# Performance work log

Measured on AMD Instinct MI355X. Metric: run time of the kernel, lower is better.

Reference implementation:

```python
import jax, jax.numpy as jnp
import numpy as np

KH, KW = 3, 3
DH, DW = 1, 1
H_OUT, W_OUT = 64, 64


def setup_inputs() -> dict:
    key = jax.random.key(0)
    k1, k2, k3 = jax.random.split(key, 3)
    x = jax.random.normal(k1, (32, 16, 66, 66), dtype=jnp.float32)
    # per-location (locally-connected) weights: [1, C_out, C_in, H_out, W_out, kh*kw]
    weight = jax.random.normal(k2, (1, 32, 16, 64, 64, 9), dtype=jnp.float32) * 0.1
    bias = jax.random.normal(k3, (1, 32, 64, 64), dtype=jnp.float32) * 0.1
    return {"x": x, "weight": weight, "bias": bias}


def _unfold(x):
    # torch x.unfold(2,kh,dh).unfold(3,kw,dw).view(B,C,Ho,Wo,kh*kw):
    # kernel index order is (i over kh, then j over kw).
    patches = jnp.stack(
        [x[:, :, i : i + H_OUT * DH : DH, j : j + W_OUT * DW : DW]
         for i in range(KH) for j in range(KW)],
        axis=-1,
    )  # [B, C_in, H_out, W_out, kh*kw]
    return patches


def reference(x, weight, bias):
    patches = _unfold(x)  # [B, C_in, Ho, Wo, K]
    # (x.unsqueeze(1) * weight).sum([2, -1]) == contraction over C_in and kernel,
    # with per-(h,w) unique weights; einsum avoids the huge 6D intermediate.
    out = jnp.einsum("bchwk,ochwk->bohw", patches, weight[0])
    out = out + bias  # bias has leading 1 batch dim, broadcasts
    return out
```

## Files before the change

kernel.cpp:

```cpp
#include <hip/hip_runtime.h>


#define CI_ 16
#define H_  64
#define W_  64
#define XW_ 66

typedef float f32x16 __attribute__((ext_vector_type(16)));
typedef short s16x8  __attribute__((ext_vector_type(8)));

__device__ inline short f2bf(float f) {
  unsigned u = __builtin_bit_cast(unsigned, f);
  u += 0x7fffu + ((u >> 16) & 1u);
  return (short)(u >> 16);
}

__device__ inline void gload_lds16(const float* g, void* l) {
  __builtin_amdgcn_global_load_lds(
      (const __attribute__((address_space(1))) void*)g,
      (__attribute__((address_space(3))) void*)l, 16, 0, 0);
}

__global__ __launch_bounds__(256) void prep_x(const float* __restrict__ x,
                                              short* __restrict__ xP) {
  const int t = blockIdx.x * 256 + threadIdx.x;
  const int oct = t & 1;
  const int b   = (t >> 1) & 31;
  const int hhww = t >> 6;
  const float* sp = x + ((size_t)b * CI_ + oct * 8) * 4356 + hhww;
  s16x8 v;
#pragma unroll
  for (int e = 0; e < 8; ++e) v[e] = f2bf(sp[(size_t)e * 4356]);
  *(s16x8*)(xP + (size_t)t * 8) = v;
}

__global__ __launch_bounds__(256) void lc2d_fused(
    const short* __restrict__ xP, const float* __restrict__ wt,
    const float* __restrict__ bias, float* __restrict__ out) {
  __shared__ float wlin[16 * 32 * 36];

  const int d = blockIdx.x;
  const int L = (d & 7) * 128 + (d >> 3);
  const int wq = L & 15;
  const int h  = L >> 4;
  const int tx = threadIdx.x;
  const int w2 = threadIdx.y;
  const int tid = w2 * 64 + tx;
  const int ln   = tx & 31;
  const int half = tx >> 5;
  const int w = wq * 4 + w2;

  const short* ap0 = xP + ln * 16 + half * 8;
  s16x8 af[9];
#pragma unroll
  for (int kk = 0; kk < 9; ++kk) {
    const int i = kk / 3, j = kk - 3 * i;
    af[kk] = *(const s16x8*)(ap0 + (size_t)((h + i) * XW_ + (w + j)) * 512);
  }

#pragma unroll
  for (int i = 0; i < 18; ++i) {
    const int G = i * 256 + tid;
    const int segL = G / 9;
    const int q    = G - 9 * segL;
    const int o = segL & 31, c = segL >> 5;
    const float* src = wt +
        (((size_t)(o * 16 + c) * 9216 + (size_t)h * 144 + wq * 9 + q) << 2);
    gload_lds16(src, (char*)wlin + (size_t)(i * 256 + w2 * 64) * 16);
  }
  __syncthreads();

  f32x16 acc = {0,0,0,0,0,0,0,0,0,0,0,0,0,0,0,0};
  const int bbase = half * 9216 + ln * 36 + w2 * 9;
#pragma unroll
  for (int kk = 0; kk < 9; ++kk) {
    s16x8 bf;
#pragma unroll
    for (int e = 0; e < 8; ++e) {
      bf[e] = f2bf(wlin[bbase + e * 1152 + kk]);
    }
    acc = __builtin_amdgcn_mfma_f32_32x32x16_bf16(af[kk], bf, acc, 0, 0, 0);
  }

  __syncthreads();
  float* tr = (float*)wlin;
#pragma unroll
  for (int r = 0; r < 16; ++r) {
    const int b = (r & 3) + 8 * (r >> 2) + 4 * half;
    tr[(w2 * 32 + b) * 32 + ln] = acc[r];
  }
  __syncthreads();

  const int o = tid & 31;
  const int brow = tid >> 5;
  const float4 bv = *(const float4*)(bias + ((size_t)o * H_ + h) * W_ + wq * 4);
#pragma unroll
  for (int it = 0; it < 4; ++it) {
    const int b = it * 8 + brow;
    float4 v;
    v.x = tr[(0 * 32 + b) * 32 + o] + bv.x;
    v.y = tr[(1 * 32 + b) * 32 + o] + bv.y;
    v.z = tr[(2 * 32 + b) * 32 + o] + bv.z;
    v.w = tr[(3 * 32 + b) * 32 + o] + bv.w;
    *(float4*)(out + ((size_t)b * 32 + o) * (H_ * W_) + h * W_ + wq * 4) = v;
  }
}

__global__ __launch_bounds__(256, 4) void lc2d_mfma0(
    const float* __restrict__ xs, const float* __restrict__ wt,
    const float* __restrict__ bias, float* __restrict__ out) {
  __shared__ float wlds[8 * 32 * 36];
  const int d = blockIdx.x;
  const int L = (d & 7) * 128 + (d >> 3);
  const int wq = L & 15;
  const int h  = L >> 4;
  const int tx = threadIdx.x;
  const int w2 = threadIdx.y;
  const int ln = tx & 31;
  const int half = tx >> 5;
  const int tid = w2 * 64 + tx;
  const int w = wq * 4 + w2;
  f32x16 acc = {0,0,0,0,0,0,0,0,0,0,0,0,0,0,0,0};
  const int bbase = ln * 36 + w2 * 9;
  size_t abase = (size_t)ln * 69696 + (size_t)h * XW_ + w;

  for (int s = 0; s < 2; ++s) {
    const int c0 = s * 8;
    __syncthreads();
#pragma unroll
    for (int i = 0; i < 9; ++i) {
      const int f4 = tid + i * 256;
      const int cc = f4 / 288;
      const int rem = f4 - cc * 288;
      const int oo = rem / 9;
      const int q = rem - oo * 9;
      const float4* src = (const float4*)wt +
          (((size_t)oo * CI_ + (c0 + cc)) * H_ + h) * 144 + (size_t)wq * 9 + q;
      ((float4*)wlds)[f4] = *src;
    }
    __syncthreads();
#pragma unroll
    for (int cc = 0; cc < 8; ++cc) {
      const int c = c0 + cc;
      const float* ap = xs + abase + (size_t)c * 4356;
      float av[8] = {0,0,0,0,0,0,0,0};
      float bvv[8] = {0,0,0,0,0,0,0,0};
      av[0] = ap[half ? (2 * XW_ + 2) : 0];
      bvv[0] = wlds[cc * 1152 + bbase + (half ? 8 : 0)];
      if (half == 0) {
#pragma unroll
        for (int e = 1; e < 8; ++e) {
          const int i = e / 3, j = e - 3 * i;
          av[e] = ap[i * XW_ + j];
          bvv[e] = wlds[cc * 1152 + bbase + e];
        }
      }
      s16x8 afr, bfr;
#pragma unroll
      for (int e = 0; e < 8; ++e) { afr[e] = f2bf(av[e]); bfr[e] = f2bf(bvv[e]); }
      acc = __builtin_amdgcn_mfma_f32_32x32x16_bf16(afr, bfr, acc, 0, 0, 0);
    }
  }
  const float bvv = bias[((size_t)ln * H_ + h) * W_ + w];
#pragma unroll
  for (int r = 0; r < 16; ++r) {
    const int b = (r & 3) + 8 * (r >> 2) + 4 * half;
    out[(((size_t)b * 32 + ln) * H_ + h) * W_ + w] = acc[r] + bvv;
  }
}

extern "C" void kernel_launch(void* const* d_in, const int* in_sizes, int n_in,
                              void* d_out, int out_size, void* d_ws, size_t ws_size,
                              hipStream_t stream) {
  const float* x    = (const float*)d_in[0];
  const float* wt   = (const float*)d_in[1];
  const float* bias = (const float*)d_in[2];
  float* out = (float*)d_out;

  const size_t xp_bytes = (size_t)66 * 66 * 32 * 16 * sizeof(short);
  if (ws_size >= xp_bytes) {
    short* xP = (short*)d_ws;
    prep_x<<<1089, 256, 0, stream>>>(x, xP);
    lc2d_fused<<<1024, dim3(64, 4, 1), 0, stream>>>(xP, wt, bias, out);
  } else {
    lc2d_mfma0<<<1024, dim3(64, 4, 1), 0, stream>>>(x, wt, bias, out);
  }
}
```

Measured before the change: 39.62 us.

## Process two output rows per block with double-buffered weight prefetch

Each block now handles two output rows (h and h+4) instead of one, and the grid is halved to match. All global and async-to-LDS loads for both rows are issued up front into two separate LDS buffers. A partial vmcnt wait then releases compute on the first row while the second row's loads are still in flight, so the second row's memory latency overlaps the first row's MFMA work and stores. In exchange LDS use roughly doubles to about 147KB per block, which limits each CU to one resident block and removes inter-block latency hiding.

```diff
diff --git a/kernel.cpp b/kernel.cpp
--- a/kernel.cpp
+++ b/kernel.cpp
@@ -37,12 +37,13 @@
 __global__ __launch_bounds__(256) void lc2d_fused(
     const short* __restrict__ xP, const float* __restrict__ wt,
     const float* __restrict__ bias, float* __restrict__ out) {
-  __shared__ float wlin[16 * 32 * 36];
+  __shared__ float pw[2][18432];
 
   const int d = blockIdx.x;
-  const int L = (d & 7) * 128 + (d >> 3);
-  const int wq = L & 15;
-  const int h  = L >> 4;
+  const int L0 = (d & 7) * 128 + (d >> 3);
+  const int wq = L0 & 15;
+  const int h0 = L0 >> 4;
+  const int h1 = h0 + 4;
   const int tx = threadIdx.x;
   const int w2 = threadIdx.y;
   const int tid = w2 * 64 + tx;
@@ -51,13 +52,14 @@
   const int w = wq * 4 + w2;
 
   const short* ap0 = xP + ln * 16 + half * 8;
-  s16x8 af[9];
+
+  s16x8 af0[9], af1[9];
 #pragma unroll
   for (int kk = 0; kk < 9; ++kk) {
     const int i = kk / 3, j = kk - 3 * i;
-    af[kk] = *(const s16x8*)(ap0 + (size_t)((h + i) * XW_ + (w + j)) * 512);
-  }
-
+    af0[kk] = *(const s16x8*)(ap0 + (size_t)((h0 + i) * XW_ + (w + j)) * 512);
+  }
+  __builtin_amdgcn_sched_barrier(0);
 #pragma unroll
   for (int i = 0; i < 18; ++i) {
     const int G = i * 256 + tid;
@@ -65,44 +67,100 @@
     const int q    = G - 9 * segL;
     const int o = segL & 31, c = segL >> 5;
     const float* src = wt +
-        (((size_t)(o * 16 + c) * 9216 + (size_t)h * 144 + wq * 9 + q) << 2);
-    gload_lds16(src, (char*)wlin + (size_t)(i * 256 + w2 * 64) * 16);
-  }
-  __syncthreads();
+        (((size_t)(o * 16 + c) * 9216 + (size_t)h0 * 144 + wq * 9 + q) << 2);
+    gload_lds16(src, (char*)&pw[0][0] + (size_t)(i * 256 + w2 * 64) * 16);
+  }
+  __builtin_amdgcn_sched_barrier(0);
+#pragma unroll
+  for (int kk = 0; kk < 9; ++kk) {
+    const int i = kk / 3, j = kk - 3 * i;
+    af1[kk] = *(const s16x8*)(ap0 + (size_t)((h1 + i) * XW_ + (w + j)) * 512);
+  }
+  __builtin_amdgcn_sched_barrier(0);
+#pragma unroll
+  for (int i = 0; i < 18; ++i) {
+    const int G = i * 256 + tid;
+    const int segL = G / 9;
+    const int q    = G - 9 * segL;
+    const int o = segL & 31, c = segL >> 5;
+    const float* src = wt +
+        (((size_t)(o * 16 + c) * 9216 + (size_t)h1 * 144 + wq * 9 + q) << 2);
+    gload_lds16(src, (char*)&pw[1][0] + (size_t)(i * 256 + w2 * 64) * 16);
+  }
+  __builtin_amdgcn_sched_barrier(0);
+
+  asm volatile("s_waitcnt vmcnt(27)" ::: "memory");
+  __builtin_amdgcn_sched_barrier(0);
+  __builtin_amdgcn_s_barrier();
+  __builtin_amdgcn_sched_barrier(0);
+
+  const int bbase = half * 9216 + ln * 36 + w2 * 9;
 
   f32x16 acc = {0,0,0,0,0,0,0,0,0,0,0,0,0,0,0,0};
-  const int bbase = half * 9216 + ln * 36 + w2 * 9;
 #pragma unroll
   for (int kk = 0; kk < 9; ++kk) {
     s16x8 bf;
 #pragma unroll
-    for (int e = 0; e < 8; ++e) {
-      bf[e] = f2bf(wlin[bbase + e * 1152 + kk]);
-    }
-    acc = __builtin_amdgcn_mfma_f32_32x32x16_bf16(af[kk], bf, acc, 0, 0, 0);
-  }
-
-  __syncthreads();
-  float* tr = (float*)wlin;
+    for (int e = 0; e < 8; ++e) bf[e] = f2bf(pw[0][bbase + e * 1152 + kk]);
+    acc = __builtin_amdgcn_mfma_f32_32x32x16_bf16(af0[kk], bf, acc, 0, 0, 0);
+  }
+
+  __syncthreads();
+
+  float* tr = &pw[0][0];
 #pragma unroll
   for (int r = 0; r < 16; ++r) {
     const int b = (r & 3) + 8 * (r >> 2) + 4 * half;
     tr[(w2 * 32 + b) * 32 + ln] = acc[r];
   }
   __syncthreads();
-
-  const int o = tid & 31;
-  const int brow = tid >> 5;
-  const float4 bv = *(const float4*)(bias + ((size_t)o * H_ + h) * W_ + wq * 4);
-#pragma unroll
-  for (int it = 0; it < 4; ++it) {
-    const int b = it * 8 + brow;
-    float4 v;
-    v.x = tr[(0 * 32 + b) * 32 + o] + bv.x;
-    v.y = tr[(1 * 32 + b) * 32 + o] + bv.y;
-    v.z = tr[(2 * 32 + b) * 32 + o] + bv.z;
-    v.w = tr[(3 * 32 + b) * 32 + o] + bv.w;
-    *(float4*)(out + ((size_t)b * 32 + o) * (H_ * W_) + h * W_ + wq * 4) = v;
+  {
+    const int o = tid & 31;
+    const int brow = tid >> 5;
+    const float4 bv = *(const float4*)(bias + ((size_t)o * H_ + h0) * W_ + wq * 4);
+#pragma unroll
+    for (int it = 0; it < 4; ++it) {
+      const int b = it * 8 + brow;
+      float4 v;
+      v.x = tr[(0 * 32 + b) * 32 + o] + bv.x;
+      v.y = tr[(1 * 32 + b) * 32 + o] + bv.y;
+      v.z = tr[(2 * 32 + b) * 32 + o] + bv.z;
+      v.w = tr[(3 * 32 + b) * 32 + o] + bv.w;
+      *(float4*)(out + ((size_t)b * 32 + o) * (H_ * W_) + h0 * W_ + wq * 4) = v;
+    }
+  }
+
+  f32x16 acc1 = {0,0,0,0,0,0,0,0,0,0,0,0,0,0,0,0};
+#pragma unroll
+  for (int kk = 0; kk < 9; ++kk) {
+    s16x8 bf;
+#pragma unroll
+    for (int e = 0; e < 8; ++e) bf[e] = f2bf(pw[1][bbase + e * 1152 + kk]);
+    acc1 = __builtin_amdgcn_mfma_f32_32x32x16_bf16(af1[kk], bf, acc1, 0, 0, 0);
+  }
+
+  __syncthreads();
+
+#pragma unroll
+  for (int r = 0; r < 16; ++r) {
+    const int b = (r & 3) + 8 * (r >> 2) + 4 * half;
+    tr[(w2 * 32 + b) * 32 + ln] = acc1[r];
+  }
+  __syncthreads();
+  {
+    const int o = tid & 31;
+    const int brow = tid >> 5;
+    const float4 bv = *(const float4*)(bias + ((size_t)o * H_ + h1) * W_ + wq * 4);
+#pragma unroll
+    for (int it = 0; it < 4; ++it) {
+      const int b = it * 8 + brow;
+      float4 v;
+      v.x = tr[(0 * 32 + b) * 32 + o] + bv.x;
+      v.y = tr[(1 * 32 + b) * 32 + o] + bv.y;
+      v.z = tr[(2 * 32 + b) * 32 + o] + bv.z;
+      v.w = tr[(3 * 32 + b) * 32 + o] + bv.w;
+      *(float4*)(out + ((size_t)b * 32 + o) * (H_ * W_) + h1 * W_ + wq * 4) = v;
+    }
   }
 }
 
@@ -181,7 +239,7 @@
   if (ws_size >= xp_bytes) {
     short* xP = (short*)d_ws;
     prep_x<<<1089, 256, 0, stream>>>(x, xP);
-    lc2d_fused<<<1024, dim3(64, 4, 1), 0, stream>>>(xP, wt, bias, out);
+    lc2d_fused<<<512, dim3(64, 4, 1), 0, stream>>>(xP, wt, bias, out);
   } else {
     lc2d_mfma0<<<1024, dim3(64, 4, 1), 0, stream>>>(x, wt, bias, out);
   }
```

After: 42.92 us. 8.3% more time.
